# Performance work log

Measured on AMD Instinct MI355X. Metric: run time of the kernel, lower is better.

## Reference

```python
import jax, jax.numpy as jnp
import numpy as np

N, E, B = 40000, 640000, 8192
IN, META, HID, OUT = 768, 6, 256, 128
NE, K, REL, NET = 4, 2, 200, 3
NL, NH, FF = 4, 4, 512


def setup_inputs():
    key = jax.random.key(0)
    keys = iter(jax.random.split(key, 64))
    def p(*shape):
        return jax.random.normal(next(keys), shape, jnp.float32) * 0.02
    return dict(
        x=jax.random.normal(next(keys), (N, IN + META), jnp.float32),
        noise=jax.random.normal(next(keys), (3, B, NE), jnp.float32),
        g_lin1_w=p(HID, IN + META), g_lin1_b=p(HID),
        conv_W=p(2, HID, HID), conv_Wr=p(2, HID, REL), conv_a=p(2, 3 * HID),
        conv_Wres=p(2, HID, HID), conv_rel=p(2, NET, REL),
        g_lin2_w=p(OUT, HID), g_lin2_b=p(OUT),
        te_w=p(OUT, IN), te_b=p(OUT),
        me_w1=p(HID, META), me_b1=p(HID), me_w2=p(OUT, HID), me_b2=p(OUT),
        moe_gate_w=p(3, NE, OUT), moe_noise_w=p(3, OUT),
        moe_w1=p(3, NE, 4 * OUT, OUT), moe_b1=p(3, NE, 4 * OUT),
        moe_w2=p(3, NE, OUT, 4 * OUT), moe_b2=p(3, NE, OUT),
        tf_qkv_w=p(NL, 3 * OUT, OUT), tf_qkv_b=p(NL, 3 * OUT),
        tf_out_w=p(NL, OUT, OUT), tf_out_b=p(NL, OUT),
        tf_ln1_g=jnp.ones((NL, OUT), jnp.float32), tf_ln1_b=jnp.zeros((NL, OUT), jnp.float32),
        tf_ff1_w=p(NL, FF, OUT), tf_ff1_b=p(NL, FF),
        tf_ff2_w=p(NL, OUT, FF), tf_ff2_b=p(NL, OUT),
        tf_ln2_g=jnp.ones((NL, OUT), jnp.float32), tf_ln2_b=jnp.zeros((NL, OUT), jnp.float32),
        clf_w=p(2, 3 * OUT), clf_b=p(2),
        edge_index=jax.random.randint(next(keys), (2, E), 0, N),
        edge_type=jax.random.randint(next(keys), (E,), 0, NET),
        batch_size=B,
    )


def _seg_softmax(logit, seg, n):
    m = jax.ops.segment_max(logit, seg, num_segments=n)
    e = jnp.exp(logit - m[seg])
    s = jax.ops.segment_sum(e, seg, num_segments=n)
    return e / (s[seg] + 1e-16)


def _hgn_layer(h, src, dst, et, W, Wr, a, Wres, rel, final):
    n, d = h.shape[0], W.shape[0]
    Wx = h @ W.T  # [N, HID]
    # a(cat(Wx_i, Wx_j, Wr_rel)) decomposed: per-node + per-edge-type scalars
    s_i = Wx @ a[:d]
    s_j = Wx @ a[d:2 * d]
    r_s = (rel @ Wr.T) @ a[2 * d:]  # [NET]
    logit = jax.nn.leaky_relu(s_i[dst] + s_j[src] + r_s[et], 0.2)
    alpha = _seg_softmax(logit, dst, n)
    agg = jax.ops.segment_sum(Wx[src] * alpha[:, None], dst, num_segments=n)
    out = jax.nn.elu(agg + h @ Wres.T)
    if final:
        out = out / jnp.maximum(jnp.linalg.norm(out, axis=1, keepdims=True), 1e-12)
    return out


def _moe(xv, eps, gate_w, noise_w, w1, b1, w2, b2):
    g = xv @ gate_w.T                       # [B, NE]
    nsd = jax.nn.softplus(xv @ noise_w)     # [B]
    h = g + eps * nsd[:, None]
    _, bot = jax.lax.top_k(-h, K)           # bottom-K experts get -inf
    drop = jnp.sum(jax.nn.one_hot(bot, NE, dtype=h.dtype), axis=1) > 0
    h = jnp.where(drop, -jnp.inf, h)
    L = jax.nn.softmax(h, axis=1)
    logits, idx = jax.lax.top_k(L, K)
    tmp = L.sum(0)
    loss = (jnp.std(tmp, ddof=1) / jnp.mean(tmp)) ** 2
    comb = jnp.einsum('bs,bse->be', logits, jax.nn.one_hot(idx, NE, dtype=L.dtype))
    h1 = jax.nn.relu(jnp.einsum('bd,ehd->ebh', xv, w1) + b1[:, None, :])
    eo = jnp.einsum('ebh,eoh->ebo', h1, w2) + b2[:, None, :]  # [NE, B, OUT]
    return jnp.einsum('be,ebo->bo', comb, eo), loss


def _ln(x, g, b):
    mu = x.mean(-1, keepdims=True)
    var = x.var(-1, keepdims=True)
    return (x - mu) / jnp.sqrt(var + 1e-5) * g + b


def _tf_layer(x, qkv_w, qkv_b, out_w, out_b, ln1g, ln1b, f1w, f1b, f2w, f2b, ln2g, ln2b):
    Bq, S, D = x.shape
    hd = D // NH
    qkv = x @ qkv_w.T + qkv_b
    q, k, v = jnp.split(qkv, 3, axis=-1)
    q = q.reshape(Bq, S, NH, hd)
    k = k.reshape(Bq, S, NH, hd)
    v = v.reshape(Bq, S, NH, hd)
    att = jax.nn.softmax(jnp.einsum('bshd,bthd->bhst', q, k) / jnp.sqrt(jnp.float32(hd)), axis=-1)
    o = jnp.einsum('bhst,bthd->bshd', att, v).reshape(Bq, S, D)
    x = _ln(x + o @ out_w.T + out_b, ln1g, ln1b)
    ff = jax.nn.relu(x @ f1w.T + f1b) @ f2w.T + f2b
    return _ln(x + ff, ln2g, ln2b)


def _forward(x, noise, g_lin1_w, g_lin1_b, conv_W, conv_Wr, conv_a, conv_Wres, conv_rel,
             g_lin2_w, g_lin2_b, te_w, te_b, me_w1, me_b1, me_w2, me_b2,
             moe_gate_w, moe_noise_w, moe_w1, moe_b1, moe_w2, moe_b2,
             tf_qkv_w, tf_qkv_b, tf_out_w, tf_out_b, tf_ln1_g, tf_ln1_b,
             tf_ff1_w, tf_ff1_b, tf_ff2_w, tf_ff2_b, tf_ln2_g, tf_ln2_b,
             clf_w, clf_b, edge_index, edge_type, batch_size):
    src, dst = edge_index[0], edge_index[1]
    # graph encoder (dropout is eval no-op)
    h = jax.nn.relu(x @ g_lin1_w.T + g_lin1_b)
    h = _hgn_layer(h, src, dst, edge_type, conv_W[0], conv_Wr[0], conv_a[0], conv_Wres[0], conv_rel[0], False)
    h = _hgn_layer(h, src, dst, edge_type, conv_W[1], conv_Wr[1], conv_a[1], conv_Wres[1], conv_rel[1], True)
    graph = jax.nn.relu(h @ g_lin2_w.T + g_lin2_b)
    x_g = graph[:batch_size]
    text = x[:batch_size, :IN]
    meta = x[:batch_size, IN:]
    x_t = jax.nn.relu(text @ te_w.T + te_b)
    x_m = jax.nn.relu(jax.nn.relu(meta @ me_w1.T + me_b1) @ me_w2.T + me_b2)
    outs, losses = [], []
    for i, xv in enumerate((x_g, x_t, x_m)):
        o, l = _moe(xv, noise[i], moe_gate_w[i], moe_noise_w[i], moe_w1[i], moe_b1[i], moe_w2[i], moe_b2[i])
        outs.append(o)
        losses.append(l)
    loss = losses[0] + losses[1] + losses[2]
    z = jnp.stack(outs, axis=1)  # [B, 3, OUT]
    for li in range(NL):
        z = _tf_layer(z, tf_qkv_w[li], tf_qkv_b[li], tf_out_w[li], tf_out_b[li],
                      tf_ln1_g[li], tf_ln1_b[li], tf_ff1_w[li], tf_ff1_b[li],
                      tf_ff2_w[li], tf_ff2_b[li], tf_ln2_g[li], tf_ln2_b[li])
    logits = z.reshape(z.shape[0], -1) @ clf_w.T + clf_b
    return logits, loss


def reference(x, noise, g_lin1_w, g_lin1_b, conv_W, conv_Wr, conv_a, conv_Wres, conv_rel,
              g_lin2_w, g_lin2_b, te_w, te_b, me_w1, me_b1, me_w2, me_b2,
              moe_gate_w, moe_noise_w, moe_w1, moe_b1, moe_w2, moe_b2,
              tf_qkv_w, tf_qkv_b, tf_out_w, tf_out_b, tf_ln1_g, tf_ln1_b,
              tf_ff1_w, tf_ff1_b, tf_ff2_w, tf_ff2_b, tf_ln2_g, tf_ln2_b,
              clf_w, clf_b, edge_index, edge_type, batch_size):
    return _forward(x, noise, g_lin1_w, g_lin1_b, conv_W, conv_Wr, conv_a, conv_Wres, conv_rel,
                    g_lin2_w, g_lin2_b, te_w, te_b, me_w1, me_b1, me_w2, me_b2,
                    moe_gate_w, moe_noise_w, moe_w1, moe_b1, moe_w2, moe_b2,
                    tf_qkv_w, tf_qkv_b, tf_out_w, tf_out_b, tf_ln1_g, tf_ln1_b,
                    tf_ff1_w, tf_ff1_b, tf_ff2_w, tf_ff2_b, tf_ln2_g, tf_ln2_b,
                    clf_w, clf_b, edge_index, edge_type, batch_size)
```

## Files before the change

### kernel.cpp

```cpp
#include <hip/hip_runtime.h>
#include <hip/hip_bf16.h>
#include <math.h>

#define NN 40000
#define EE 640000
#define BB 8192
#define IN_DIM 768
#define META_DIM 6
#define XDIM 774
#define HID 256
#define OUT_D 128
#define NEXP 4
#define NET_T 3
#define REL_D 200
#define NLAY 4
#define FF_D 512

typedef __attribute__((ext_vector_type(8))) short short8;
typedef __attribute__((ext_vector_type(4))) float f32x4;

__device__ __forceinline__ ushort f2bf(float f) {
    union { float f; unsigned u; } a; a.f = f;
    unsigned u = a.u;
    unsigned r = (u + 0x7FFFu + ((u >> 16) & 1u)) >> 16;
    return (ushort)r;
}
__device__ __forceinline__ float bf2f(ushort h) {
    union { unsigned u; float f; } a; a.u = ((unsigned)h) << 16;
    return a.f;
}
__device__ __forceinline__ unsigned packsplit(float v) {
    ushort h = f2bf(v);
    ushort lo = f2bf(v - bf2f(h));
    return ((unsigned)h << 16) | lo;
}

__global__ void cvt_pack_kernel(const float* __restrict__ src, int ldsrc, int Kreal,
                                unsigned* __restrict__ pk, int R, int ldp)
{
    size_t i = (size_t)blockIdx.x * blockDim.x + threadIdx.x;
    size_t total = (size_t)R * ldp;
    if (i >= total) return;
    int col = (int)(i % ldp);
    int row = (int)(i / ldp);
    float v = (col < Kreal) ? src[(size_t)row * ldsrc + col] : 0.f;
    pk[i] = packsplit(v);
}

static void cvt_pack(const float* src, int ldsrc, int Kreal, unsigned* pk,
                     int R, int ldp, hipStream_t s)
{
    size_t total = (size_t)R * ldp;
    cvt_pack_kernel<<<(int)((total + 255) / 256), 256, 0, s>>>(src, ldsrc, Kreal, pk, R, ldp);
}

template<int ACT, int HAS_RES, int OUT_SPLIT, int B_PACKED>
__global__ __launch_bounds__(256) void mfma3_128(
    const unsigned* __restrict__ Ap, int lda,
    const void* __restrict__ Bp, int ldb,
    const float* __restrict__ bias, const float* __restrict__ res,
    float* __restrict__ C, unsigned* __restrict__ Cpk,
    int M, int Nn, int K)
{
    __shared__ __align__(16) ushort Ash[128 * 40];
    __shared__ __align__(16) ushort Asl[128 * 40];
    __shared__ __align__(16) ushort Bsh[128 * 40];
    __shared__ __align__(16) ushort Bsl[128 * 40];

    const float*    Bf = (const float*)Bp;
    const unsigned* Bk = (const unsigned*)Bp;

    int bn = blockIdx.x * 128;
    int bm = blockIdx.y * 128;
    int t = threadIdx.x;
    int wave = t >> 6, lane = t & 63;
    int wm = wave & 1, wn = wave >> 1;
    int quad = lane >> 4, r = lane & 15;

    int arow0 = t >> 2,           ac80 = t & 3;
    int arow1 = (t + 256) >> 2,   ac81 = t & 3;

    uint4 apre[2][2];
    uint4 bprek[2][2];
    float4 bpref[2][2];

    auto loadA = [&](int k0) {
        int g0 = bm + arow0; if (g0 > M - 1) g0 = M - 1;
        int g1 = bm + arow1; if (g1 > M - 1) g1 = M - 1;
        const unsigned* p0 = Ap + (size_t)g0 * lda + k0 + ac80 * 8;
        const unsigned* p1 = Ap + (size_t)g1 * lda + k0 + ac81 * 8;
        apre[0][0] = *(const uint4*)p0; apre[0][1] = *(const uint4*)(p0 + 4);
        apre[1][0] = *(const uint4*)p1; apre[1][1] = *(const uint4*)(p1 + 4);
    };
    auto loadB = [&](int k0) {
        if (B_PACKED) {
            const unsigned* p0 = Bk + (size_t)(bn + arow0) * ldb + k0 + ac80 * 8;
            const unsigned* p1 = Bk + (size_t)(bn + arow1) * ldb + k0 + ac81 * 8;
            bprek[0][0] = *(const uint4*)p0; bprek[0][1] = *(const uint4*)(p0 + 4);
            bprek[1][0] = *(const uint4*)p1; bprek[1][1] = *(const uint4*)(p1 + 4);
        } else {
            const float* p0 = Bf + (size_t)(bn + arow0) * ldb + k0 + ac80 * 8;
            const float* p1 = Bf + (size_t)(bn + arow1) * ldb + k0 + ac81 * 8;
            bpref[0][0] = *(const float4*)p0; bpref[0][1] = *(const float4*)(p0 + 4);
            bpref[1][0] = *(const float4*)p1; bpref[1][1] = *(const float4*)(p1 + 4);
        }
    };
    auto storeTiles = [&]() {
#pragma unroll
        for (int i = 0; i < 2; i++) {
            int row = i ? arow1 : arow0, c8 = i ? ac81 : ac80;
            unsigned u[8] = {apre[i][0].x, apre[i][0].y, apre[i][0].z, apre[i][0].w,
                             apre[i][1].x, apre[i][1].y, apre[i][1].z, apre[i][1].w};
            short8 hi, lo;
#pragma unroll
            for (int e = 0; e < 8; e++) { hi[e] = (short)(u[e] >> 16); lo[e] = (short)(u[e] & 0xFFFFu); }
            *(short8*)&Ash[row * 40 + c8 * 8] = hi;
            *(short8*)&Asl[row * 40 + c8 * 8] = lo;
        }
#pragma unroll
        for (int i = 0; i < 2; i++) {
            int row = i ? arow1 : arow0, c8 = i ? ac81 : ac80;
            short8 hi, lo;
            if (B_PACKED) {
                unsigned u[8] = {bprek[i][0].x, bprek[i][0].y, bprek[i][0].z, bprek[i][0].w,
                                 bprek[i][1].x, bprek[i][1].y, bprek[i][1].z, bprek[i][1].w};
#pragma unroll
                for (int e = 0; e < 8; e++) { hi[e] = (short)(u[e] >> 16); lo[e] = (short)(u[e] & 0xFFFFu); }
            } else {
                float f[8] = {bpref[i][0].x, bpref[i][0].y, bpref[i][0].z, bpref[i][0].w,
                              bpref[i][1].x, bpref[i][1].y, bpref[i][1].z, bpref[i][1].w};
#pragma unroll
                for (int e = 0; e < 8; e++) {
                    ushort h = f2bf(f[e]);
                    hi[e] = (short)h;
                    lo[e] = (short)f2bf(f[e] - bf2f(h));
                }
            }
            *(short8*)&Bsh[row * 40 + c8 * 8] = hi;
            *(short8*)&Bsl[row * 40 + c8 * 8] = lo;
        }
    };

    f32x4 acc[4][4];
#pragma unroll
    for (int i = 0; i < 4; i++)
#pragma unroll
        for (int j = 0; j < 4; j++) acc[i][j] = (f32x4){0.f, 0.f, 0.f, 0.f};

    loadA(0); loadB(0);
    for (int k0 = 0; k0 < K; k0 += 32) {
        storeTiles();
        __syncthreads();
        if (k0 + 32 < K) { loadA(k0 + 32); loadB(k0 + 32); }

        short8 ah[4], al[4];
#pragma unroll
        for (int i = 0; i < 4; i++) {
            int ro = (wm * 64 + i * 16 + r) * 40 + quad * 8;
            ah[i] = *(const short8*)&Ash[ro];
            al[i] = *(const short8*)&Asl[ro];
        }
#pragma unroll
        for (int j = 0; j < 4; j++) {
            int ro = (wn * 64 + j * 16 + r) * 40 + quad * 8;
            short8 bh = *(const short8*)&Bsh[ro];
            short8 bl = *(const short8*)&Bsl[ro];
#pragma unroll
            for (int i = 0; i < 4; i++)
                acc[i][j] = __builtin_amdgcn_mfma_f32_16x16x32_bf16(ah[i], bh, acc[i][j], 0, 0, 0);
#pragma unroll
            for (int i = 0; i < 4; i++)
                acc[i][j] = __builtin_amdgcn_mfma_f32_16x16x32_bf16(ah[i], bl, acc[i][j], 0, 0, 0);
#pragma unroll
            for (int i = 0; i < 4; i++)
                acc[i][j] = __builtin_amdgcn_mfma_f32_16x16x32_bf16(al[i], bh, acc[i][j], 0, 0, 0);
        }
        __syncthreads();
    }

#pragma unroll
    for (int j = 0; j < 4; j++) {
        int col = bn + wn * 64 + j * 16 + r;
        float bc = bias ? bias[col] : 0.f;
#pragma unroll
        for (int i = 0; i < 4; i++) {
#pragma unroll
            for (int reg = 0; reg < 4; reg++) {
                int row = bm + wm * 64 + i * 16 + quad * 4 + reg;
                if (row >= M) continue;
                float v = acc[i][j][reg] + bc;
                if (HAS_RES) v += res[(size_t)row * Nn + col];
                if (ACT == 1) v = fmaxf(v, 0.f);
                else if (ACT == 2) v = (v > 0.f) ? v : expm1f(v);
                if (OUT_SPLIT) Cpk[(size_t)row * Nn + col] = packsplit(v);
                else           C[(size_t)row * Nn + col] = v;
            }
        }
    }
}

template<int ACT, int HAS_RES, int OUT_SPLIT, int B_PACKED>
static void m128_launch(const unsigned* Ap, int lda, const void* Bp, int ldb,
                        const float* bias, const float* res,
                        float* C, unsigned* Cpk,
                        int M, int Nn, int K, hipStream_t s)
{
    dim3 grid(Nn / 128, (M + 127) / 128);
    mfma3_128<ACT, HAS_RES, OUT_SPLIT, B_PACKED><<<grid, 256, 0, s>>>(
        Ap, lda, Bp, ldb, bias, res, C, Cpk, M, Nn, K);
}

template<int ACT>
__global__ void gemm_kernel(const float* __restrict__ A, int lda,
                            const float* __restrict__ Bw,
                            const float* __restrict__ bias,
                            const float* __restrict__ res,
                            float* __restrict__ C, int M, int Nn, int K)
{
    __shared__ float As[16][68];
    __shared__ float Bs[16][68];
    int bm = blockIdx.y * 64, bn = blockIdx.x * 64;
    int t = threadIdx.x;
    int tx = t & 15, ty = t >> 4;
    float acc[4][4] = {{0.f}};

    for (int k0 = 0; k0 < K; k0 += 16) {
#pragma unroll
        for (int i = 0; i < 4; i++) {
            int l = t * 4 + i; int mm = l >> 4, kk = l & 15;
            int gm = bm + mm, gk = k0 + kk;
            As[kk][mm] = (gm < M && gk < K) ? A[(size_t)gm * lda + gk] : 0.f;
        }
#pragma unroll
        for (int i = 0; i < 4; i++) {
            int l = t * 4 + i; int nn = l >> 4, kk = l & 15;
            int gn = bn + nn, gk = k0 + kk;
            Bs[kk][nn] = (gn < Nn && gk < K) ? Bw[(size_t)gn * K + gk] : 0.f;
        }
        __syncthreads();
#pragma unroll
        for (int kk = 0; kk < 16; kk++) {
            float4 a4 = *reinterpret_cast<const float4*>(&As[kk][ty * 4]);
            float4 b4 = *reinterpret_cast<const float4*>(&Bs[kk][tx * 4]);
            float a0[4] = {a4.x, a4.y, a4.z, a4.w};
            float b0[4] = {b4.x, b4.y, b4.z, b4.w};
#pragma unroll
            for (int i = 0; i < 4; i++)
#pragma unroll
                for (int j = 0; j < 4; j++)
                    acc[i][j] += a0[i] * b0[j];
        }
        __syncthreads();
    }
#pragma unroll
    for (int i = 0; i < 4; i++) {
        int gm = bm + ty * 4 + i; if (gm >= M) continue;
#pragma unroll
        for (int j = 0; j < 4; j++) {
            int gn = bn + tx * 4 + j; if (gn >= Nn) continue;
            float v = acc[i][j];
            if (bias) v += bias[gn];
            if (res)  v += res[(size_t)gm * Nn + gn];
            if (ACT == 1) v = fmaxf(v, 0.f);
            else if (ACT == 2) v = (v > 0.f) ? v : expm1f(v);
            C[(size_t)gm * Nn + gn] = v;
        }
    }
}

static void launch_gemm(int act, const float* A, int lda, const float* Bw,
                        const float* bias, const float* res, float* C,
                        int M, int Nn, int K, hipStream_t s)
{
    dim3 grid((Nn + 63) / 64, (M + 63) / 64);
    if (act == 1) gemm_kernel<1><<<grid, 256, 0, s>>>(A, lda, Bw, bias, res, C, M, Nn, K);
    else          gemm_kernel<0><<<grid, 256, 0, s>>>(A, lda, Bw, bias, res, C, M, Nn, K);
}

template<int ACT, int A_BF16, int OUT_BF16>
__global__ __launch_bounds__(256) void mfma_gemm(
    const void* __restrict__ Ap, size_t strideAz,
    const float* __restrict__ Bw, size_t strideBz,
    const float* __restrict__ bias, size_t strideBiasz,
    void* __restrict__ Cp, size_t strideCz,
    int M, int Nn, int K)
{
    __shared__ __align__(16) ushort As[128 * 40];
    __shared__ __align__(16) ushort Bs[64 * 40];

    int z = blockIdx.z;
    const float*  Af  = (const float*)Ap  + (A_BF16 ? 0 : z * strideAz);
    const ushort* Ab  = (const ushort*)Ap + (A_BF16 ? z * strideAz : 0);
    const float*  Bwz = Bw + z * strideBz;
    const float*  bz  = bias ? bias + z * strideBiasz : nullptr;
    float*  Cf = (float*)Cp  + (OUT_BF16 ? 0 : z * strideCz);
    ushort* Cb = (ushort*)Cp + (OUT_BF16 ? z * strideCz : 0);

    int bn = blockIdx.x * 64;
    int bm = blockIdx.y * 128;
    int t = threadIdx.x;
    int wave = t >> 6, lane = t & 63;
    int wm = wave & 1, wn = wave >> 1;
    int quad = lane >> 4, r = lane & 15;

    int ar0 = t >> 2, ac0 = t & 3;
    int ar1 = (t + 256) >> 2;
    int br = t >> 2, bc = t & 3;

    short8 apre_b[2];
    float4 apre_f[4];
    float4 bpre[2];

    auto loadA = [&](int k0) {
        if (A_BF16) {
            apre_b[0] = *(const short8*)(Ab + (size_t)(bm + ar0) * K + k0 + ac0 * 8);
            apre_b[1] = *(const short8*)(Ab + (size_t)(bm + ar1) * K + k0 + ac0 * 8);
        } else {
#pragma unroll
            for (int i = 0; i < 4; i++) {
                int idx = t + i * 256;
                int row = idx >> 3, c4 = idx & 7;
                apre_f[i] = *(const float4*)(Af + (size_t)(bm + row) * K + k0 + c4 * 4);
            }
        }
    };
    auto loadB = [&](int k0) {
        const float* p = Bwz + (size_t)(bn + br) * K + k0 + bc * 8;
        bpre[0] = *(const float4*)p;
        bpre[1] = *(const float4*)(p + 4);
    };
    auto storeTiles = [&]() {
        if (A_BF16) {
            *(short8*)&As[ar0 * 40 + ac0 * 8] = apre_b[0];
            *(short8*)&As[ar1 * 40 + ac0 * 8] = apre_b[1];
        } else {
#pragma unroll
            for (int i = 0; i < 4; i++) {
                int idx = t + i * 256;
                int row = idx >> 3, c4 = idx & 7;
                ushort4 u;
                u.x = f2bf(apre_f[i].x); u.y = f2bf(apre_f[i].y);
                u.z = f2bf(apre_f[i].z); u.w = f2bf(apre_f[i].w);
                *(ushort4*)&As[row * 40 + c4 * 4] = u;
            }
        }
        {
            float f[8] = {bpre[0].x, bpre[0].y, bpre[0].z, bpre[0].w,
                          bpre[1].x, bpre[1].y, bpre[1].z, bpre[1].w};
            short8 hb;
#pragma unroll
            for (int e = 0; e < 8; e++) hb[e] = (short)f2bf(f[e]);
            *(short8*)&Bs[br * 40 + bc * 8] = hb;
        }
    };

    f32x4 acc[4][2];
#pragma unroll
    for (int i = 0; i < 4; i++)
#pragma unroll
        for (int j = 0; j < 2; j++) acc[i][j] = (f32x4){0.f, 0.f, 0.f, 0.f};

    loadA(0); loadB(0);
    for (int k0 = 0; k0 < K; k0 += 32) {
        storeTiles();
        __syncthreads();
        if (k0 + 32 < K) { loadA(k0 + 32); loadB(k0 + 32); }

        short8 af[4];
#pragma unroll
        for (int i = 0; i < 4; i++)
            af[i] = *(const short8*)&As[(wm * 64 + i * 16 + r) * 40 + quad * 8];
#pragma unroll
        for (int j = 0; j < 2; j++) {
            short8 bf = *(const short8*)&Bs[(wn * 32 + j * 16 + r) * 40 + quad * 8];
#pragma unroll
            for (int i = 0; i < 4; i++)
                acc[i][j] = __builtin_amdgcn_mfma_f32_16x16x32_bf16(af[i], bf, acc[i][j], 0, 0, 0);
        }
        __syncthreads();
    }

    float bcol[2];
#pragma unroll
    for (int j = 0; j < 2; j++)
        bcol[j] = bz ? bz[bn + wn * 32 + j * 16 + r] : 0.f;
#pragma unroll
    for (int i = 0; i < 4; i++) {
#pragma unroll
        for (int j = 0; j < 2; j++) {
            int col = bn + wn * 32 + j * 16 + r;
#pragma unroll
            for (int reg = 0; reg < 4; reg++) {
                int row = bm + wm * 64 + i * 16 + quad * 4 + reg;
                float v = acc[i][j][reg] + bcol[j];
                if (ACT == 1) v = fmaxf(v, 0.f);
                if (OUT_BF16) Cb[(size_t)row * Nn + col] = f2bf(v);
                else          Cf[(size_t)row * Nn + col] = v;
            }
        }
    }
}

template<int ACT, int A_BF16, int OUT_BF16>
static void mfma_launch(const void* A, size_t sAz, const float* Bw, size_t sBz,
                        const float* bias, size_t sbz, void* C, size_t sCz,
                        int M, int Nn, int K, int batch, hipStream_t s)
{
    dim3 grid(Nn / 64, M / 128, batch);
    mfma_gemm<ACT, A_BF16, OUT_BF16><<<grid, 256, 0, s>>>(A, sAz, Bw, sBz, bias, sbz, C, sCz, M, Nn, K);
}

__global__ void sisj_kernel(const float* __restrict__ Wx, const float* __restrict__ a,
                            float* __restrict__ s_i, float* __restrict__ s_j, int n)
{
    int t = threadIdx.x; int w = t >> 6, l = t & 63;
    int m = blockIdx.x * 4 + w; if (m >= n) return;
    const float* r = Wx + (size_t)m * HID;
    float v1 = 0.f, v2 = 0.f;
#pragma unroll
    for (int i = 0; i < 4; i++) {
        float xv = r[l + 64 * i];
        v1 += xv * a[l + 64 * i];
        v2 += xv * a[HID + l + 64 * i];
    }
    for (int off = 32; off; off >>= 1) { v1 += __shfl_down(v1, off); v2 += __shfl_down(v2, off); }
    if (l == 0) { s_i[m] = v1; s_j[m] = v2; }
}

__global__ void rs_kernel(const float* __restrict__ Wr, const float* __restrict__ rel,
                          const float* __restrict__ a3, float* __restrict__ rs)
{
    __shared__ float red[256];
    int tt = blockIdx.x; int j = threadIdx.x;
    const float* relr = rel + tt * REL_D;
    const float* wr = Wr + (size_t)j * REL_D;
    float wsum = 0.f;
    for (int k = 0; k < REL_D; k++) wsum += wr[k] * relr[k];
    red[j] = wsum * a3[j];
    __syncthreads();
    for (int s2 = 128; s2; s2 >>= 1) { if (j < s2) red[j] += red[j + s2]; __syncthreads(); }
    if (j == 0) rs[tt] = red[0];
}

__global__ void deg_kernel(const int* __restrict__ dst, int* __restrict__ deg)
{
    int e = blockIdx.x * blockDim.x + threadIdx.x;
    if (e < EE) atomicAdd(&deg[dst[e]], 1);
}

__global__ void scan_kernel(const int* __restrict__ deg, int* __restrict__ rowstart,
                            int* __restrict__ cursor, int n)
{
    __shared__ int bs[1024];
    int t = threadIdx.x;
    int base = t * 40;
    int loc[40];
    int sum = 0;
#pragma unroll
    for (int i = 0; i < 40; i++) {
        int v = (base + i < n) ? deg[base + i] : 0;
        loc[i] = sum; sum += v;
    }
    bs[t] = sum;
    __syncthreads();
    for (int off = 1; off < 1024; off <<= 1) {
        int x = (t >= off) ? bs[t - off] : 0;
        __syncthreads();
        bs[t] += x;
        __syncthreads();
    }
    int excl = bs[t] - sum;
#pragma unroll
    for (int i = 0; i < 40; i++) {
        if (base + i < n) { int v = excl + loc[i]; rowstart[base + i] = v; cursor[base + i] = v; }
    }
    if (t == 1023) rowstart[n] = bs[1023];
}

__global__ void fill_kernel(const int* __restrict__ src, const int* __restrict__ dst,
                            const int* __restrict__ et, int* __restrict__ cursor,
                            unsigned* __restrict__ csr_val)
{
    int e = blockIdx.x * blockDim.x + threadIdx.x;
    if (e >= EE) return;
    int d = dst[e];
    int pos = atomicAdd(&cursor[d], 1);
    csr_val[pos] = (unsigned)src[e] | ((unsigned)et[e] << 16);
}

__global__ void csr_agg_kernel(const unsigned* __restrict__ csr_val,
                               const int* __restrict__ rowstart,
                               const float* __restrict__ s_i, const float* __restrict__ s_j,
                               const float* __restrict__ rsv,
                               const float* __restrict__ Wx, float* __restrict__ agg)
{
    int t = threadIdx.x; int w = t >> 6, l = t & 63;
    int node = blockIdx.x * 4 + w; if (node >= NN) return;
    int start = rowstart[node], end = rowstart[node + 1];
    float r0 = rsv[0], r1 = rsv[1], r2 = rsv[2];
    float si = s_i[node];

    float m = -INFINITY;
    for (int i = start + l; i < end; i += 64) {
        unsigned v = csr_val[i];
        int s = v & 0xFFFF; int et = v >> 16;
        float rr = (et == 0) ? r0 : ((et == 1) ? r1 : r2);
        float lg = si + s_j[s] + rr;
        lg = (lg >= 0.f) ? lg : 0.2f * lg;
        m = fmaxf(m, lg);
    }
    for (int off = 32; off; off >>= 1) m = fmaxf(m, __shfl_down(m, off));
    m = __shfl(m, 0);

    float a0 = 0.f, a1 = 0.f, a2 = 0.f, a3 = 0.f, ssum = 0.f;
    for (int c = start; c < end; c += 64) {
        int nchunk = min(64, end - c);
        float wgt = 0.f; int sidx = 0;
        if (l < nchunk) {
            unsigned v = csr_val[c + l];
            sidx = v & 0xFFFF; int et = v >> 16;
            float rr = (et == 0) ? r0 : ((et == 1) ? r1 : r2);
            float lg = si + s_j[sidx] + rr;
            lg = (lg >= 0.f) ? lg : 0.2f * lg;
            wgt = expf(lg - m);
            ssum += wgt;
        }
        int j = 0;
        for (; j + 4 <= nchunk; j += 4) {
            float w0 = __shfl(wgt, j),     w1 = __shfl(wgt, j + 1);
            float w2 = __shfl(wgt, j + 2), w3 = __shfl(wgt, j + 3);
            int s0 = __shfl(sidx, j),     s1 = __shfl(sidx, j + 1);
            int s2 = __shfl(sidx, j + 2), s3 = __shfl(sidx, j + 3);
            const float* p0 = Wx + (size_t)s0 * HID + l;
            const float* p1 = Wx + (size_t)s1 * HID + l;
            const float* p2 = Wx + (size_t)s2 * HID + l;
            const float* p3 = Wx + (size_t)s3 * HID + l;
            float v00 = p0[0], v01 = p0[64], v02 = p0[128], v03 = p0[192];
            float v10 = p1[0], v11 = p1[64], v12 = p1[128], v13 = p1[192];
            float v20 = p2[0], v21 = p2[64], v22 = p2[128], v23 = p2[192];
            float v30 = p3[0], v31 = p3[64], v32 = p3[128], v33 = p3[192];
            a0 += w0 * v00 + w1 * v10 + w2 * v20 + w3 * v30;
            a1 += w0 * v01 + w1 * v11 + w2 * v21 + w3 * v31;
            a2 += w0 * v02 + w1 * v12 + w2 * v22 + w3 * v32;
            a3 += w0 * v03 + w1 * v13 + w2 * v23 + w3 * v33;
        }
        for (; j < nchunk; j++) {
            float wj = __shfl(wgt, j);
            int sj = __shfl(sidx, j);
            const float* wr = Wx + (size_t)sj * HID + l;
            a0 += wj * wr[0];
            a1 += wj * wr[64];
            a2 += wj * wr[128];
            a3 += wj * wr[192];
        }
    }
    for (int off = 32; off; off >>= 1) ssum += __shfl_down(ssum, off);
    ssum = __shfl(ssum, 0);
    float inv = 1.f / (ssum + 1e-16f);
    float* ar = agg + (size_t)node * HID;
    ar[l] = a0 * inv; ar[l + 64] = a1 * inv; ar[l + 128] = a2 * inv; ar[l + 192] = a3 * inv;
}

__global__ void rownorm_pack(unsigned* __restrict__ pk, int n)
{
    int t = threadIdx.x; int w = t >> 6, l = t & 63;
    int m = blockIdx.x * 4 + w; if (m >= n) return;
    size_t base = (size_t)m * HID;
    float vals[4]; float q = 0.f;
#pragma unroll
    for (int i = 0; i < 4; i++) {
        unsigned u = pk[base + l + 64 * i];
        vals[i] = bf2f((ushort)(u >> 16)) + bf2f((ushort)(u & 0xFFFFu));
        q += vals[i] * vals[i];
    }
    for (int off = 32; off; off >>= 1) q += __shfl_down(q, off);
    q = __shfl(q, 0);
    float inv = 1.f / fmaxf(sqrtf(q), 1e-12f);
#pragma unroll
    for (int i = 0; i < 4; i++)
        pk[base + l + 64 * i] = packsplit(vals[i] * inv);
// ... 151 lines not shown
    for (int off = 32; off; off >>= 1) { v0 += __shfl_down(v0, off); v1 += __shfl_down(v1, off); }
    if (l == 0) { out[row * 2] = v0 + b[0]; out[row * 2 + 1] = v1 + b[1]; }
}

extern "C" void kernel_launch(void* const* d_in, const int* in_sizes, int n_in,
                              void* d_out, int out_size, void* d_ws, size_t ws_size,
                              hipStream_t stream)
{
    const float* x         = (const float*)d_in[0];
    const float* noise     = (const float*)d_in[1];
    const float* g_lin1_w  = (const float*)d_in[2];
    const float* g_lin1_b  = (const float*)d_in[3];
    const float* conv_W    = (const float*)d_in[4];
    const float* conv_Wr   = (const float*)d_in[5];
    const float* conv_a    = (const float*)d_in[6];
    const float* conv_Wres = (const float*)d_in[7];
    const float* conv_rel  = (const float*)d_in[8];
    const float* g_lin2_w  = (const float*)d_in[9];
    const float* g_lin2_b  = (const float*)d_in[10];
    const float* te_w      = (const float*)d_in[11];
    const float* te_b      = (const float*)d_in[12];
    const float* me_w1     = (const float*)d_in[13];
    const float* me_b1     = (const float*)d_in[14];
    const float* me_w2     = (const float*)d_in[15];
    const float* me_b2     = (const float*)d_in[16];
    const float* moe_gate_w  = (const float*)d_in[17];
    const float* moe_noise_w = (const float*)d_in[18];
    const float* moe_w1    = (const float*)d_in[19];
    const float* moe_b1    = (const float*)d_in[20];
    const float* moe_w2    = (const float*)d_in[21];
    const float* moe_b2    = (const float*)d_in[22];
    const float* tf_qkv_w  = (const float*)d_in[23];
    const float* tf_qkv_b  = (const float*)d_in[24];
    const float* tf_out_w  = (const float*)d_in[25];
    const float* tf_out_b  = (const float*)d_in[26];
    const float* tf_ln1_g  = (const float*)d_in[27];
    const float* tf_ln1_b  = (const float*)d_in[28];
    const float* tf_ff1_w  = (const float*)d_in[29];
    const float* tf_ff1_b  = (const float*)d_in[30];
    const float* tf_ff2_w  = (const float*)d_in[31];
    const float* tf_ff2_b  = (const float*)d_in[32];
    const float* tf_ln2_g  = (const float*)d_in[33];
    const float* tf_ln2_b  = (const float*)d_in[34];
    const float* clf_w     = (const float*)d_in[35];
    const float* clf_b     = (const float*)d_in[36];
    const int*   edge_index = (const int*)d_in[37];
    const int*   edge_type  = (const int*)d_in[38];

    float* ws = (float*)d_ws;

    const size_t F_A = 0;
    const size_t F_B = 10240000;
    const size_t F_C = 22822912;
    const size_t F_D = 33062912;
    const size_t F_M = 43302912;
    const size_t F_X = 44200000;

    unsigned* hApk = (unsigned*)(ws + F_A);
    float* qkv    = ws + F_A;
    float* wx     = ws + F_B;
    float* graph  = ws + F_B;
    ushort* ff1bf = (ushort*)(ws + F_B);
    float* agg    = ws + F_C;
    float* x_mh   = ws + F_C;
    ushort* h1bf  = (ushort*)(ws + F_C);
    float* attn_o = ws + F_C;
    float* tmp1   = ws + F_C + 3200000;
    unsigned* hBpk = (unsigned*)(ws + F_D);
    float* z      = ws + F_D;
    float* x_t    = ws + F_D + 3200000;
    float* x_m    = ws + F_D + 4300000;
    float* eo     = ws + F_D + 5400000;

    float* s_i    = ws + F_M;
    float* s_j    = ws + F_M + 40000;
    float* rsv    = ws + F_M + 80000;
    float* comb   = ws + F_M + 80016;
    float* tmpsum = ws + F_M + 112784;
    int* deg      = (int*)(ws + F_M + 120000);
    int* rowstart = (int*)(ws + F_M + 161000);
    int* cursor   = (int*)(ws + F_M + 202000);
    unsigned* csr_val = (unsigned*)(ws + F_M + 242000);

    unsigned* xpk  = (unsigned*)(ws + F_X);
    unsigned* wpk  = (unsigned*)(ws + F_X + 32000000);
    unsigned* mhpk = (unsigned*)(ws + F_X + 32300000);

    const int* srcv = edge_index;
    const int* dstv = edge_index + EE;

    hipMemsetAsync(deg, 0, NN * sizeof(int), stream);
    deg_kernel<<<(EE + 255) / 256, 256, 0, stream>>>(dstv, deg);
    scan_kernel<<<1, 1024, 0, stream>>>(deg, rowstart, cursor, NN);
    fill_kernel<<<(EE + 255) / 256, 256, 0, stream>>>(srcv, dstv, edge_type, cursor, csr_val);

    cvt_pack(x, XDIM, XDIM, xpk, NN, 800, stream);
    cvt_pack(g_lin1_w, XDIM, XDIM, wpk, HID, 800, stream);
    m128_launch<1, 0, 1, 1>(xpk, 800, wpk, 800, g_lin1_b, nullptr,
                            nullptr, hApk, NN, HID, 800, stream);

    unsigned *inpk = hApk, *outpk = hBpk;
    for (int layer = 0; layer < 2; layer++) {
        const float* W    = conv_W    + (size_t)layer * HID * HID;
        const float* Wr   = conv_Wr   + (size_t)layer * HID * REL_D;
        const float* a    = conv_a    + (size_t)layer * 3 * HID;
        const float* Wres = conv_Wres + (size_t)layer * HID * HID;
        const float* rel  = conv_rel  + (size_t)layer * NET_T * REL_D;

        m128_launch<0, 0, 0, 0>(inpk, HID, W, HID, nullptr, nullptr,
                                wx, nullptr, NN, HID, HID, stream);
        sisj_kernel<<<NN / 4, 256, 0, stream>>>(wx, a, s_i, s_j, NN);
        rs_kernel<<<NET_T, 256, 0, stream>>>(Wr, rel, a + 2 * HID, rsv);
        csr_agg_kernel<<<NN / 4, 256, 0, stream>>>(csr_val, rowstart, s_i, s_j, rsv, wx, agg);
        m128_launch<2, 1, 1, 0>(inpk, HID, Wres, HID, nullptr, agg,
                                nullptr, outpk, NN, HID, HID, stream);
        unsigned* tp = inpk; inpk = outpk; outpk = tp;
    }
    rownorm_pack<<<NN / 4, 256, 0, stream>>>(inpk, NN);

    m128_launch<1, 0, 0, 0>(inpk, HID, g_lin2_w, HID, g_lin2_b, nullptr,
                            graph, nullptr, NN, OUT_D, HID, stream);

    m128_launch<1, 0, 0, 0>(xpk, 800, te_w, IN_DIM, te_b, nullptr,
                            x_t, nullptr, BB, OUT_D, IN_DIM, stream);
    launch_gemm(1, x + IN_DIM, XDIM, me_w1, me_b1, nullptr, x_mh, BB, HID, META_DIM, stream);
    cvt_pack(x_mh, HID, HID, mhpk, BB, HID, stream);
    m128_launch<1, 0, 0, 0>(mhpk, HID, me_w2, HID, me_b2, nullptr,
                            x_m, nullptr, BB, OUT_D, HID, stream);

    hipMemsetAsync(tmpsum, 0, 16 * sizeof(float), stream);
    const float* xvs[3] = { graph, x_t, x_m };
    for (int v = 0; v < 3; v++) {
        const float* xv = xvs[v];
        moe_gate_kernel<<<BB / 4, 256, 0, stream>>>(
            xv, moe_gate_w + (size_t)v * NEXP * OUT_D, moe_noise_w + (size_t)v * OUT_D,
            noise + (size_t)v * BB * NEXP, comb, tmpsum + v * 4);
        mfma_launch<1, 0, 1>(xv, 0,
                             moe_w1 + (size_t)v * 4 * FF_D * OUT_D, (size_t)FF_D * OUT_D,
                             moe_b1 + (size_t)v * 4 * FF_D, FF_D,
                             h1bf, (size_t)BB * FF_D,
                             BB, FF_D, OUT_D, 4, stream);
        mfma_launch<0, 1, 0>(h1bf, (size_t)BB * FF_D,
                             moe_w2 + (size_t)v * 4 * OUT_D * FF_D, (size_t)OUT_D * FF_D,
                             moe_b2 + (size_t)v * 4 * OUT_D, OUT_D,
                             eo, (size_t)BB * OUT_D,
                             BB, OUT_D, FF_D, 4, stream);
        moe_combine_kernel<<<(BB * OUT_D) / 256, 256, 0, stream>>>(eo, comb, z + v * OUT_D);
    }

    const int MT = BB * 3;
    for (int li = 0; li < NLAY; li++) {
        mfma_launch<0, 0, 0>(z, 0, tf_qkv_w + (size_t)li * 384 * 128, 0,
                             tf_qkv_b + li * 384, 0, qkv, 0, MT, 384, 128, 1, stream);
        attn_kernel<<<(BB * 4) / 8, 256, 0, stream>>>(qkv, attn_o);
        mfma_launch<0, 0, 0>(attn_o, 0, tf_out_w + (size_t)li * 128 * 128, 0,
                             tf_out_b + li * 128, 0, tmp1, 0, MT, 128, 128, 1, stream);
        ln_residual_kernel<<<MT / 4, 256, 0, stream>>>(z, tmp1, tf_ln1_g + li * 128, tf_ln1_b + li * 128, MT);
        mfma_launch<1, 0, 1>(z, 0, tf_ff1_w + (size_t)li * 512 * 128, 0,
                             tf_ff1_b + li * 512, 0, ff1bf, 0, MT, 512, 128, 1, stream);
        mfma_launch<0, 1, 0>(ff1bf, 0, tf_ff2_w + (size_t)li * 128 * 512, 0,
                             tf_ff2_b + li * 128, 0, tmp1, 0, MT, 128, 512, 1, stream);
        ln_residual_kernel<<<MT / 4, 256, 0, stream>>>(z, tmp1, tf_ln2_g + li * 128, tf_ln2_b + li * 128, MT);
    }

    clf_kernel<<<BB / 4, 256, 0, stream>>>(z, clf_w, clf_b, (float*)d_out);
    loss_kernel<<<1, 64, 0, stream>>>(tmpsum, (float*)d_out + BB * 2);
}
```

Before: 1.719 ms.

## Restrict final GNN layer to batch rows, fuse fp32 A conversion into GEMM

The second HGN layer's aggregation and residual GEMM, the row norm and lin2 now run only over the first B nodes, since only those rows are consumed downstream. The first-layer GEMM loads fp32 x directly and splits it to bf16 hi/lo in-kernel, which removes the separate pack pass over x and its workspace buffer. GEMM tiles shrink to 64-wide N with BM a template parameter, so the smaller launches get more blocks. The cost is less data reuse per block and more redundant global loads of A and B.

```diff
diff --git a/kernel.cpp b/kernel.cpp
--- a/kernel.cpp
+++ b/kernel.cpp
@@ -54,81 +54,107 @@
     cvt_pack_kernel<<<(int)((total + 255) / 256), 256, 0, s>>>(src, ldsrc, Kreal, pk, R, ldp);
 }
 
-template<int ACT, int HAS_RES, int OUT_SPLIT, int B_PACKED>
-__global__ __launch_bounds__(256) void mfma3_128(
-    const unsigned* __restrict__ Ap, int lda,
+template<int WM, int ACT, int HAS_RES, int OUT_SPLIT, int A_FP32, int B_PACKED>
+__global__ __launch_bounds__(256) void mfma3k(
+    const void* __restrict__ Ap, int lda, int Kreal,
     const void* __restrict__ Bp, int ldb,
     const float* __restrict__ bias, const float* __restrict__ res,
     float* __restrict__ C, unsigned* __restrict__ Cpk,
     int M, int Nn, int K)
 {
-    __shared__ __align__(16) ushort Ash[128 * 40];
-    __shared__ __align__(16) ushort Asl[128 * 40];
-    __shared__ __align__(16) ushort Bsh[128 * 40];
-    __shared__ __align__(16) ushort Bsl[128 * 40];
-
+    const int BM = 32 * WM;
+    __shared__ __align__(16) ushort Ash[BM * 40];
+    __shared__ __align__(16) ushort Asl[BM * 40];
+    __shared__ __align__(16) ushort Bsh[64 * 40];
+    __shared__ __align__(16) ushort Bsl[64 * 40];
+
+    const unsigned* Ak = (const unsigned*)Ap;
+    const float*    Af = (const float*)Ap;
+    const unsigned* Bk = (const unsigned*)Bp;
     const float*    Bf = (const float*)Bp;
-    const unsigned* Bk = (const unsigned*)Bp;
-
-    int bn = blockIdx.x * 128;
-    int bm = blockIdx.y * 128;
+
+    int bn = blockIdx.x * 64;
+    int bm = blockIdx.y * BM;
     int t = threadIdx.x;
     int wave = t >> 6, lane = t & 63;
     int wm = wave & 1, wn = wave >> 1;
     int quad = lane >> 4, r = lane & 15;
 
-    int arow0 = t >> 2,           ac80 = t & 3;
-    int arow1 = (t + 256) >> 2,   ac81 = t & 3;
-
-    uint4 apre[2][2];
-    uint4 bprek[2][2];
-    float4 bpref[2][2];
+    const int ACH = (BM * 4) / 256;
+
+    uint4 apk[2][2];
+    float afp[2][8];
+    uint4 bpk[2];
+    float4 bfp[2];
 
     auto loadA = [&](int k0) {
-        int g0 = bm + arow0; if (g0 > M - 1) g0 = M - 1;
-        int g1 = bm + arow1; if (g1 > M - 1) g1 = M - 1;
-        const unsigned* p0 = Ap + (size_t)g0 * lda + k0 + ac80 * 8;
-        const unsigned* p1 = Ap + (size_t)g1 * lda + k0 + ac81 * 8;
-        apre[0][0] = *(const uint4*)p0; apre[0][1] = *(const uint4*)(p0 + 4);
-        apre[1][0] = *(const uint4*)p1; apre[1][1] = *(const uint4*)(p1 + 4);
+#pragma unroll
+        for (int i = 0; i < ACH; i++) {
+            int idx = t + i * 256;
+            int row = idx >> 2, c8 = idx & 3;
+            int grow = bm + row; if (grow > M - 1) grow = M - 1;
+            if (A_FP32) {
+                int cb = k0 + c8 * 8;
+                const float* p = Af + (size_t)grow * lda + cb;
+                if (cb + 8 <= Kreal) {
+                    float2 f0 = *(const float2*)p,     f1 = *(const float2*)(p + 2);
+                    float2 f2 = *(const float2*)(p + 4), f3 = *(const float2*)(p + 6);
+                    afp[i][0] = f0.x; afp[i][1] = f0.y; afp[i][2] = f1.x; afp[i][3] = f1.y;
+                    afp[i][4] = f2.x; afp[i][5] = f2.y; afp[i][6] = f3.x; afp[i][7] = f3.y;
+                } else {
+#pragma unroll
+                    for (int e = 0; e < 8; e++)
+                        afp[i][e] = (cb + e < Kreal) ? p[e] : 0.f;
+                }
+            } else {
+                const unsigned* p = Ak + (size_t)grow * lda + k0 + c8 * 8;
+                apk[i][0] = *(const uint4*)p; apk[i][1] = *(const uint4*)(p + 4);
+            }
+        }
     };
     auto loadB = [&](int k0) {
+        int row = t >> 2, c8 = t & 3;
         if (B_PACKED) {
-            const unsigned* p0 = Bk + (size_t)(bn + arow0) * ldb + k0 + ac80 * 8;
-            const unsigned* p1 = Bk + (size_t)(bn + arow1) * ldb + k0 + ac81 * 8;
-            bprek[0][0] = *(const uint4*)p0; bprek[0][1] = *(const uint4*)(p0 + 4);
-            bprek[1][0] = *(const uint4*)p1; bprek[1][1] = *(const uint4*)(p1 + 4);
+            const unsigned* p = Bk + (size_t)(bn + row) * ldb + k0 + c8 * 8;
+            bpk[0] = *(const uint4*)p; bpk[1] = *(const uint4*)(p + 4);
         } else {
-            const float* p0 = Bf + (size_t)(bn + arow0) * ldb + k0 + ac80 * 8;
-            const float* p1 = Bf + (size_t)(bn + arow1) * ldb + k0 + ac81 * 8;
-            bpref[0][0] = *(const float4*)p0; bpref[0][1] = *(const float4*)(p0 + 4);
-            bpref[1][0] = *(const float4*)p1; bpref[1][1] = *(const float4*)(p1 + 4);
+            const float* p = Bf + (size_t)(bn + row) * ldb + k0 + c8 * 8;
+            bfp[0] = *(const float4*)p; bfp[1] = *(const float4*)(p + 4);
         }
     };
     auto storeTiles = [&]() {
 #pragma unroll
-        for (int i = 0; i < 2; i++) {
-            int row = i ? arow1 : arow0, c8 = i ? ac81 : ac80;
-            unsigned u[8] = {apre[i][0].x, apre[i][0].y, apre[i][0].z, apre[i][0].w,
-                             apre[i][1].x, apre[i][1].y, apre[i][1].z, apre[i][1].w};
+        for (int i = 0; i < ACH; i++) {
+            int idx = t + i * 256;
+            int row = idx >> 2, c8 = idx & 3;
             short8 hi, lo;
-#pragma unroll
-            for (int e = 0; e < 8; e++) { hi[e] = (short)(u[e] >> 16); lo[e] = (short)(u[e] & 0xFFFFu); }
+            if (A_FP32) {
+#pragma unroll
+                for (int e = 0; e < 8; e++) {
+                    ushort h = f2bf(afp[i][e]);
+                    hi[e] = (short)h;
+                    lo[e] = (short)f2bf(afp[i][e] - bf2f(h));
+                }
+            } else {
+                unsigned u[8] = {apk[i][0].x, apk[i][0].y, apk[i][0].z, apk[i][0].w,
+                                 apk[i][1].x, apk[i][1].y, apk[i][1].z, apk[i][1].w};
+#pragma unroll
+                for (int e = 0; e < 8; e++) { hi[e] = (short)(u[e] >> 16); lo[e] = (short)(u[e] & 0xFFFFu); }
+            }
             *(short8*)&Ash[row * 40 + c8 * 8] = hi;
             *(short8*)&Asl[row * 40 + c8 * 8] = lo;
         }
-#pragma unroll
-        for (int i = 0; i < 2; i++) {
-            int row = i ? arow1 : arow0, c8 = i ? ac81 : ac80;
+        {
+            int row = t >> 2, c8 = t & 3;
             short8 hi, lo;
             if (B_PACKED) {
-                unsigned u[8] = {bprek[i][0].x, bprek[i][0].y, bprek[i][0].z, bprek[i][0].w,
-                                 bprek[i][1].x, bprek[i][1].y, bprek[i][1].z, bprek[i][1].w};
+                unsigned u[8] = {bpk[0].x, bpk[0].y, bpk[0].z, bpk[0].w,
+                                 bpk[1].x, bpk[1].y, bpk[1].z, bpk[1].w};
 #pragma unroll
                 for (int e = 0; e < 8; e++) { hi[e] = (short)(u[e] >> 16); lo[e] = (short)(u[e] & 0xFFFFu); }
             } else {
-                float f[8] = {bpref[i][0].x, bpref[i][0].y, bpref[i][0].z, bpref[i][0].w,
-                              bpref[i][1].x, bpref[i][1].y, bpref[i][1].z, bpref[i][1].w};
+                float f[8] = {bfp[0].x, bfp[0].y, bfp[0].z, bfp[0].w,
+                              bfp[1].x, bfp[1].y, bfp[1].z, bfp[1].w};
 #pragma unroll
                 for (int e = 0; e < 8; e++) {
                     ushort h = f2bf(f[e]);
@@ -141,11 +167,11 @@
         }
     };
 
-    f32x4 acc[4][4];
-#pragma unroll
-    for (int i = 0; i < 4; i++)
-#pragma unroll
-        for (int j = 0; j < 4; j++) acc[i][j] = (f32x4){0.f, 0.f, 0.f, 0.f};
+    f32x4 acc[WM][2];
+#pragma unroll
+    for (int i = 0; i < WM; i++)
+#pragma unroll
+        for (int j = 0; j < 2; j++) acc[i][j] = (f32x4){0.f, 0.f, 0.f, 0.f};
 
     loadA(0); loadB(0);
     for (int k0 = 0; k0 < K; k0 += 32) {
@@ -153,40 +179,40 @@
         __syncthreads();
         if (k0 + 32 < K) { loadA(k0 + 32); loadB(k0 + 32); }
 
-        short8 ah[4], al[4];
-#pragma unroll
-        for (int i = 0; i < 4; i++) {
-            int ro = (wm * 64 + i * 16 + r) * 40 + quad * 8;
+        short8 ah[WM], al[WM];
+#pragma unroll
+        for (int i = 0; i < WM; i++) {
+            int ro = (wm * (WM * 16) + i * 16 + r) * 40 + quad * 8;
             ah[i] = *(const short8*)&Ash[ro];
             al[i] = *(const short8*)&Asl[ro];
         }
 #pragma unroll
-        for (int j = 0; j < 4; j++) {
-            int ro = (wn * 64 + j * 16 + r) * 40 + quad * 8;
+        for (int j = 0; j < 2; j++) {
+            int ro = (wn * 32 + j * 16 + r) * 40 + quad * 8;
             short8 bh = *(const short8*)&Bsh[ro];
             short8 bl = *(const short8*)&Bsl[ro];
 #pragma unroll
-            for (int i = 0; i < 4; i++)
+            for (int i = 0; i < WM; i++)
                 acc[i][j] = __builtin_amdgcn_mfma_f32_16x16x32_bf16(ah[i], bh, acc[i][j], 0, 0, 0);
 #pragma unroll
-            for (int i = 0; i < 4; i++)
+            for (int i = 0; i < WM; i++)
                 acc[i][j] = __builtin_amdgcn_mfma_f32_16x16x32_bf16(ah[i], bl, acc[i][j], 0, 0, 0);
 #pragma unroll
-            for (int i = 0; i < 4; i++)
+            for (int i = 0; i < WM; i++)
                 acc[i][j] = __builtin_amdgcn_mfma_f32_16x16x32_bf16(al[i], bh, acc[i][j], 0, 0, 0);
         }
         __syncthreads();
     }
 
 #pragma unroll
-    for (int j = 0; j < 4; j++) {
-        int col = bn + wn * 64 + j * 16 + r;
+    for (int j = 0; j < 2; j++) {
+        int col = bn + wn * 32 + j * 16 + r;
         float bc = bias ? bias[col] : 0.f;
 #pragma unroll
-        for (int i = 0; i < 4; i++) {
+        for (int i = 0; i < WM; i++) {
 #pragma unroll
             for (int reg = 0; reg < 4; reg++) {
-                int row = bm + wm * 64 + i * 16 + quad * 4 + reg;
+                int row = bm + wm * (WM * 16) + i * 16 + quad * 4 + reg;
                 if (row >= M) continue;
                 float v = acc[i][j][reg] + bc;
                 if (HAS_RES) v += res[(size_t)row * Nn + col];
@@ -199,15 +225,16 @@
     }
 }
 
-template<int ACT, int HAS_RES, int OUT_SPLIT, int B_PACKED>
-static void m128_launch(const unsigned* Ap, int lda, const void* Bp, int ldb,
-                        const float* bias, const float* res,
-                        float* C, unsigned* Cpk,
-                        int M, int Nn, int K, hipStream_t s)
-{
-    dim3 grid(Nn / 128, (M + 127) / 128);
-    mfma3_128<ACT, HAS_RES, OUT_SPLIT, B_PACKED><<<grid, 256, 0, s>>>(
-        Ap, lda, Bp, ldb, bias, res, C, Cpk, M, Nn, K);
+template<int WM, int ACT, int HAS_RES, int OUT_SPLIT, int A_FP32, int B_PACKED>
+static void m3_launch(const void* Ap, int lda, int Kreal, const void* Bp, int ldb,
+                      const float* bias, const float* res,
+                      float* C, unsigned* Cpk,
+                      int M, int Nn, int K, hipStream_t s)
+{
+    const int BM = 32 * WM;
+    dim3 grid(Nn / 64, (M + BM - 1) / BM);
+    mfma3k<WM, ACT, HAS_RES, OUT_SPLIT, A_FP32, B_PACKED><<<grid, 256, 0, s>>>(
+        Ap, lda, Kreal, Bp, ldb, bias, res, C, Cpk, M, Nn, K);
 }
 
 template<int ACT>
@@ -262,19 +289,9 @@
             if (bias) v += bias[gn];
             if (res)  v += res[(size_t)gm * Nn + gn];
             if (ACT == 1) v = fmaxf(v, 0.f);
-            else if (ACT == 2) v = (v > 0.f) ? v : expm1f(v);
             C[(size_t)gm * Nn + gn] = v;
         }
     }
-}
-
-static void launch_gemm(int act, const float* A, int lda, const float* Bw,
-                        const float* bias, const float* res, float* C,
-                        int M, int Nn, int K, hipStream_t s)
-{
-    dim3 grid((Nn + 63) / 64, (M + 63) / 64);
-    if (act == 1) gemm_kernel<1><<<grid, 256, 0, s>>>(A, lda, Bw, bias, res, C, M, Nn, K);
-    else          gemm_kernel<0><<<grid, 256, 0, s>>>(A, lda, Bw, bias, res, C, M, Nn, K);
 }
 
 template<int ACT, int A_BF16, int OUT_BF16>
@@ -285,7 +302,7 @@
     void* __restrict__ Cp, size_t strideCz,
     int M, int Nn, int K)
 {
-    __shared__ __align__(16) ushort As[128 * 40];
+    __shared__ __align__(16) ushort As[64 * 40];
     __shared__ __align__(16) ushort Bs[64 * 40];
 
     int z = blockIdx.z;
@@ -297,27 +314,23 @@
     ushort* Cb = (ushort*)Cp + (OUT_BF16 ? z * strideCz : 0);
 
     int bn = blockIdx.x * 64;
-    int bm = blockIdx.y * 128;
+    int bm = blockIdx.y * 64;
     int t = threadIdx.x;
     int wave = t >> 6, lane = t & 63;
     int wm = wave & 1, wn = wave >> 1;
     int quad = lane >> 4, r = lane & 15;
 
-    int ar0 = t >> 2, ac0 = t & 3;
-    int ar1 = (t + 256) >> 2;
-    int br = t >> 2, bc = t & 3;
-
-    short8 apre_b[2];
-    float4 apre_f[4];
+    short8 apre_b;
+    float4 apre_f[2];
     float4 bpre[2];
+    int ar = t >> 2, ac = t & 3;
 
     auto loadA = [&](int k0) {
         if (A_BF16) {
-            apre_b[0] = *(const short8*)(Ab + (size_t)(bm + ar0) * K + k0 + ac0 * 8);
-            apre_b[1] = *(const short8*)(Ab + (size_t)(bm + ar1) * K + k0 + ac0 * 8);
+            apre_b = *(const short8*)(Ab + (size_t)(bm + ar) * K + k0 + ac * 8);
         } else {
 #pragma unroll
-            for (int i = 0; i < 4; i++) {
+            for (int i = 0; i < 2; i++) {
                 int idx = t + i * 256;
                 int row = idx >> 3, c4 = idx & 7;
                 apre_f[i] = *(const float4*)(Af + (size_t)(bm + row) * K + k0 + c4 * 4);
@@ -325,17 +338,16 @@
         }
     };
     auto loadB = [&](int k0) {
-        const float* p = Bwz + (size_t)(bn + br) * K + k0 + bc * 8;
+        const float* p = Bwz + (size_t)(bn + ar) * K + k0 + ac * 8;
         bpre[0] = *(const float4*)p;
         bpre[1] = *(const float4*)(p + 4);
     };
     auto storeTiles = [&]() {
         if (A_BF16) {
-            *(short8*)&As[ar0 * 40 + ac0 * 8] = apre_b[0];
-            *(short8*)&As[ar1 * 40 + ac0 * 8] = apre_b[1];
+            *(short8*)&As[ar * 40 + ac * 8] = apre_b;
         } else {
 #pragma unroll
-            for (int i = 0; i < 4; i++) {
+            for (int i = 0; i < 2; i++) {
                 int idx = t + i * 256;
                 int row = idx >> 3, c4 = idx & 7;
                 ushort4 u;
@@ -350,13 +362,13 @@
             short8 hb;
 #pragma unroll
             for (int e = 0; e < 8; e++) hb[e] = (short)f2bf(f[e]);
-            *(short8*)&Bs[br * 40 + bc * 8] = hb;
+            *(short8*)&Bs[ar * 40 + ac * 8] = hb;
         }
     };
 
-    f32x4 acc[4][2];
-#pragma unroll
-    for (int i = 0; i < 4; i++)
+    f32x4 acc[2][2];
+#pragma unroll
+    for (int i = 0; i < 2; i++)
 #pragma unroll
         for (int j = 0; j < 2; j++) acc[i][j] = (f32x4){0.f, 0.f, 0.f, 0.f};
 
@@ -366,33 +378,30 @@
         __syncthreads();
         if (k0 + 32 < K) { loadA(k0 + 32); loadB(k0 + 32); }
 
-        short8 af[4];
-#pragma unroll
-        for (int i = 0; i < 4; i++)
-            af[i] = *(const short8*)&As[(wm * 64 + i * 16 + r) * 40 + quad * 8];
+        short8 af[2];
+#pragma unroll
+        for (int i = 0; i < 2; i++)
+            af[i] = *(const short8*)&As[(wm * 32 + i * 16 + r) * 40 + quad * 8];
 #pragma unroll
         for (int j = 0; j < 2; j++) {
             short8 bf = *(const short8*)&Bs[(wn * 32 + j * 16 + r) * 40 + quad * 8];
 #pragma unroll
-            for (int i = 0; i < 4; i++)
+            for (int i = 0; i < 2; i++)
                 acc[i][j] = __builtin_amdgcn_mfma_f32_16x16x32_bf16(af[i], bf, acc[i][j], 0, 0, 0);
         }
         __syncthreads();
     }
 
-    float bcol[2];
-#pragma unroll
-    for (int j = 0; j < 2; j++)
-        bcol[j] = bz ? bz[bn + wn * 32 + j * 16 + r] : 0.f;
-#pragma unroll
-    for (int i = 0; i < 4; i++) {
-#pragma unroll
-        for (int j = 0; j < 2; j++) {
-            int col = bn + wn * 32 + j * 16 + r;
+#pragma unroll
+    for (int j = 0; j < 2; j++) {
+        int col = bn + wn * 32 + j * 16 + r;
+        float bc = bz ? bz[col] : 0.f;
+#pragma unroll
+        for (int i = 0; i < 2; i++) {
 #pragma unroll
             for (int reg = 0; reg < 4; reg++) {
-                int row = bm + wm * 64 + i * 16 + quad * 4 + reg;
-                float v = acc[i][j][reg] + bcol[j];
+                int row = bm + wm * 32 + i * 16 + quad * 4 + reg;
+                float v = acc[i][j][reg] + bc;
                 if (ACT == 1) v = fmaxf(v, 0.f);
                 if (OUT_BF16) Cb[(size_t)row * Nn + col] = f2bf(v);
                 else          Cf[(size_t)row * Nn + col] = v;
@@ -406,7 +415,7 @@
                         const float* bias, size_t sbz, void* C, size_t sCz,
                         int M, int Nn, int K, int batch, hipStream_t s)
 {
-    dim3 grid(Nn / 64, M / 128, batch);
+    dim3 grid(Nn / 64, M / 64, batch);
     mfma_gemm<ACT, A_BF16, OUT_BF16><<<grid, 256, 0, s>>>(A, sAz, Bw, sBz, bias, sbz, C, sCz, M, Nn, K);
 }
 
@@ -492,10 +501,11 @@
                                const int* __restrict__ rowstart,
                                const float* __restrict__ s_i, const float* __restrict__ s_j,
                                const float* __restrict__ rsv,
-                               const float* __restrict__ Wx, float* __restrict__ agg)
+                               const float* __restrict__ Wx, float* __restrict__ agg,
+                               int nlim)
 {
     int t = threadIdx.x; int w = t >> 6, l = t & 63;
-    int node = blockIdx.x * 4 + w; if (node >= NN) return;
+    int node = blockIdx.x * 4 + w; if (node >= nlim) return;
     int start = rowstart[node], end = rowstart[node + 1];
     float r0 = rsv[0], r1 = rsv[1], r2 = rsv[2];
     float si = s_i[node];
@@ -813,9 +823,7 @@
     int* cursor   = (int*)(ws + F_M + 202000);
     unsigned* csr_val = (unsigned*)(ws + F_M + 242000);
 
-    unsigned* xpk  = (unsigned*)(ws + F_X);
-    unsigned* wpk  = (unsigned*)(ws + F_X + 32000000);
-    unsigned* mhpk = (unsigned*)(ws + F_X + 32300000);
+    unsigned* wpk  = (unsigned*)(ws + F_X);
 
     const int* srcv = edge_index;
     const int* dstv = edge_index + EE;
@@ -825,10 +833,9 @@
     scan_kernel<<<1, 1024, 0, stream>>>(deg, rowstart, cursor, NN);
     fill_kernel<<<(EE + 255) / 256, 256, 0, stream>>>(srcv, dstv, edge_type, cursor, csr_val);
 
-    cvt_pack(x, XDIM, XDIM, xpk, NN, 800, stream);
     cvt_pack(g_lin1_w, XDIM, XDIM, wpk, HID, 800, stream);
-    m128_launch<1, 0, 1, 1>(xpk, 800, wpk, 800, g_lin1_b, nullptr,
-                            nullptr, hApk, NN, HID, 800, stream);
+    m3_launch<4, 1, 0, 1, 1, 1>(x, XDIM, XDIM, wpk, 800, g_lin1_b, nullptr,
+                                nullptr, hApk, NN, HID, 800, stream);
 
     unsigned *inpk = hApk, *outpk = hBpk;
     for (int layer = 0; layer < 2; layer++) {
@@ -837,27 +844,35 @@
         const float* a    = conv_a    + (size_t)layer * 3 * HID;
         const float* Wres = conv_Wres + (size_t)layer * HID * HID;
         const float* rel  = conv_rel  + (size_t)layer * NET_T * REL_D;
-
-        m128_launch<0, 0, 0, 0>(inpk, HID, W, HID, nullptr, nullptr,
-                                wx, nullptr, NN, HID, HID, stream);
+        int mOut = (layer == 1) ? BB : NN;
+
+        m3_launch<4, 0, 0, 0, 0, 0>(inpk, HID, HID, W, HID, nullptr, nullptr,
+                                    wx, nullptr, NN, HID, HID, stream);
         sisj_kernel<<<NN / 4, 256, 0, stream>>>(wx, a, s_i, s_j, NN);
         rs_kernel<<<NET_T, 256, 0, stream>>>(Wr, rel, a + 2 * HID, rsv);
-        csr_agg_kernel<<<NN / 4, 256, 0, stream>>>(csr_val, rowstart, s_i, s_j, rsv, wx, agg);
-        m128_launch<2, 1, 1, 0>(inpk, HID, Wres, HID, nullptr, agg,
-                                nullptr, outpk, NN, HID, HID, stream);
+        csr_agg_kernel<<<(mOut + 3) / 4, 256, 0, stream>>>(csr_val, rowstart, s_i, s_j, rsv, wx, agg, mOut);
+        if (layer == 0)
+            m3_launch<4, 2, 1, 1, 0, 0>(inpk, HID, HID, Wres, HID, nullptr, agg,
+                                        nullptr, outpk, mOut, HID, HID, stream);
+        else
+            m3_launch<2, 2, 1, 1, 0, 0>(inpk, HID, HID, Wres, HID, nullptr, agg,
+                                        nullptr, outpk, mOut, HID, HID, stream);
         unsigned* tp = inpk; inpk = outpk; outpk = tp;
     }
-    rownorm_pack<<<NN / 4, 256, 0, stream>>>(inpk, NN);
-
-    m128_launch<1, 0, 0, 0>(inpk, HID, g_lin2_w, HID, g_lin2_b, nullptr,
-                            graph, nullptr, NN, OUT_D, HID, stream);
-
-    m128_launch<1, 0, 0, 0>(xpk, 800, te_w, IN_DIM, te_b, nullptr,
-                            x_t, nullptr, BB, OUT_D, IN_DIM, stream);
-    launch_gemm(1, x + IN_DIM, XDIM, me_w1, me_b1, nullptr, x_mh, BB, HID, META_DIM, stream);
-    cvt_pack(x_mh, HID, HID, mhpk, BB, HID, stream);
-    m128_launch<1, 0, 0, 0>(mhpk, HID, me_w2, HID, me_b2, nullptr,
-                            x_m, nullptr, BB, OUT_D, HID, stream);
+    rownorm_pack<<<BB / 4, 256, 0, stream>>>(inpk, BB);
+
+    m3_launch<2, 1, 0, 0, 0, 0>(inpk, HID, HID, g_lin2_w, HID, g_lin2_b, nullptr,
+                                graph, nullptr, BB, OUT_D, HID, stream);
+
+    m3_launch<2, 1, 0, 0, 1, 0>(x, XDIM, IN_DIM, te_w, IN_DIM, te_b, nullptr,
+                                x_t, nullptr, BB, OUT_D, IN_DIM, stream);
+    {
+        dim3 g((HID + 63) / 64, (BB + 63) / 64);
+        gemm_kernel<1><<<g, 256, 0, stream>>>(x + IN_DIM, XDIM, me_w1, me_b1, nullptr,
+                                              x_mh, BB, HID, META_DIM);
+    }
+    m3_launch<2, 1, 0, 0, 1, 0>(x_mh, HID, HID, me_w2, HID, me_b2, nullptr,
+                                x_m, nullptr, BB, OUT_D, HID, stream);
 
     hipMemsetAsync(tmpsum, 0, 16 * sizeof(float), stream);
     const float* xvs[3] = { graph, x_t, x_m };
```

Measured after the change: 1.521 ms. 11.5% less time.
